# Performance work log

Hardware: AMD Instinct MI355X
Metric: run time of the kernel (lower is better)

The kernel has to match this reference:

```python
import jax, jax.numpy as jnp
import numpy as np

B, S, D = 32, 2048, 1024   # batch, seq, attention_in_dim
A = 1024                   # attention_dim
CTX = 1024                 # attention_context_dim
ADD = 256                  # additional decoder input dim
H = 1024                   # hidden_dim
OUT = 1024                 # output_dim
DEC_IN = 2 * D + ADD


def setup_inputs() -> dict:
    key = jax.random.key(0)
    ks = jax.random.split(key, 24)
    sc = 0.03
    inp = {
        "encoded_seq_ours": jax.random.normal(ks[0], (B, S, D), jnp.float32),
        "encoded_seq_ours_len": jax.random.randint(ks[1], (B,), 1, S + 1),
        "encoded_seq_theirs": jax.random.normal(ks[2], (B, S, D), jnp.float32),
        "encoded_seq_theirs_len": jax.random.randint(ks[3], (B,), 1, S + 1),
        "attention_context": jax.random.normal(ks[4], (B, CTX), jnp.float32),
        "additional_decoder_input": jax.random.normal(ks[5], (B, ADD), jnp.float32),
        "h0": jax.random.normal(ks[6], (B, H), jnp.float32),
        "c0": jax.random.normal(ks[7], (B, H), jnp.float32),
        "h1": jax.random.normal(ks[8], (B, H), jnp.float32),
        "c1": jax.random.normal(ks[9], (B, H), jnp.float32),
        "hidden_idx": jnp.arange(B, dtype=jnp.int32),
        # attention_theirs params (the module uses attention_theirs for BOTH calls)
        "att_Wh": jax.random.normal(ks[10], (A, D), jnp.float32) * sc,
        "att_Wc": jax.random.normal(ks[11], (A, CTX), jnp.float32) * sc,
        "att_v": jax.random.normal(ks[12], (1, A), jnp.float32) * sc,
        # LSTMCell layer 0
        "Wih0": jax.random.normal(ks[13], (4 * H, DEC_IN), jnp.float32) * sc,
        "Whh0": jax.random.normal(ks[14], (4 * H, H), jnp.float32) * sc,
        "bih0": jnp.zeros((4 * H,), jnp.float32),
        "bhh0": jnp.zeros((4 * H,), jnp.float32),
        # LSTMCell layer 1
        "Wih1": jax.random.normal(ks[15], (4 * H, H), jnp.float32) * sc,
        "Whh1": jax.random.normal(ks[16], (4 * H, H), jnp.float32) * sc,
        "bih1": jnp.zeros((4 * H,), jnp.float32),
        "bhh1": jnp.zeros((4 * H,), jnp.float32),
        # output linear (+ tanh activation)
        "Wout": jax.random.normal(ks[17], (OUT, H), jnp.float32) * sc,
        "bout": jnp.zeros((OUT,), jnp.float32),
    }
    return inp


def _attention(history, context, lengths, Wh, Wc, v):
    # history: [B,S,D], context: [B,CTX], lengths: [B]
    seq = history.shape[1]
    ha = jnp.einsum('bsd,ad->bsa', history, Wh)          # [B,S,A]
    ca = (context @ Wc.T)[:, None, :]                    # [B,1,A]
    score = jnp.einsum('bsa,oa->bso', jnp.tanh(ha + ca), v)  # [B,S,1]
    mask = (jnp.arange(seq) >= lengths[:, None])[:, :, None]  # [B,S,1] True = pad
    score = jnp.where(mask, -jnp.inf, score)
    score = jax.nn.softmax(score, axis=1)
    score = jnp.where(mask, 0.0, score)
    att = jnp.einsum('bs,bsd->bd', score[..., 0], history)    # [B,D]
    return att, score


def _lstm_cell(x, h, c, Wih, Whh, bih, bhh):
    gates = x @ Wih.T + h @ Whh.T + bih + bhh   # [B,4H]
    i, f, g, o = jnp.split(gates, 4, axis=-1)    # torch gate order: i,f,g,o
    i, f, o = jax.nn.sigmoid(i), jax.nn.sigmoid(f), jax.nn.sigmoid(o)
    g = jnp.tanh(g)
    c_new = f * c + i * g
    h_new = o * jnp.tanh(c_new)
    return h_new, c_new


def reference(encoded_seq_ours, encoded_seq_ours_len, encoded_seq_theirs,
              encoded_seq_theirs_len, attention_context, additional_decoder_input,
              h0, c0, h1, c1, hidden_idx,
              att_Wh, att_Wc, att_v,
              Wih0, Whh0, bih0, bhh0, Wih1, Whh1, bih1, bhh1, Wout, bout):
    # NOTE: original module uses attention_theirs for BOTH attention calls
    # (attention_ours is constructed but never used) -- reproduced faithfully.
    encoded_att_ours, scores_ours = _attention(
        encoded_seq_theirs, attention_context, encoded_seq_theirs_len,
        att_Wh, att_Wc, att_v)
    encoded_att_theirs, scores_theirs = _attention(
        encoded_seq_ours, attention_context, encoded_seq_ours_len,
        att_Wh, att_Wc, att_v)
    x = jnp.concatenate([encoded_att_ours, encoded_att_theirs,
                         additional_decoder_input], axis=-1)

    # layer 0 (dropout is eval-mode identity)
    h0_sel, c0_sel = h0[hidden_idx], c0[hidden_idx]
    h0_out, c0_out = _lstm_cell(x, h0_sel, c0_sel, Wih0, Whh0, bih0, bhh0)
    h0_new = h0.at[hidden_idx].set(h0_out)
    c0_new = c0.at[hidden_idx].set(c0_out)

    # layer 1
    h1_sel, c1_sel = h1[hidden_idx], c1[hidden_idx]
    h1_out, c1_out = _lstm_cell(h0_out, h1_sel, c1_sel, Wih1, Whh1, bih1, bhh1)
    h1_new = h1.at[hidden_idx].set(h1_out)
    c1_new = c1.at[hidden_idx].set(c1_out)

    out = jnp.tanh(h1_out @ Wout.T + bout)  # activation='tanh'
    return (out, h0_new, c0_new, h1_new, c1_new, scores_ours, scores_theirs)
```

## Files before the change

### kernel.cpp

```cpp
#include <hip/hip_runtime.h>
#include <hip/hip_bf16.h>

typedef __bf16 bf16x8 __attribute__((ext_vector_type(8)));
typedef float  f32x16 __attribute__((ext_vector_type(16)));
typedef unsigned short ushort_t;

#define B_   32
#define S_   2048
#define D_   1024
#define A_   1024
#define ADD_ 256
#define H_   1024

__device__ __forceinline__ float fast_rcp(float x){ return __builtin_amdgcn_rcpf(x); }
__device__ __forceinline__ float fast_sig(float x){ return fast_rcp(1.f + __expf(-x)); }
__device__ __forceinline__ float fast_tanh(float x){
  float ax = fabsf(x);
  float e  = __expf(-2.f * ax);
  float t  = (1.f - e) * fast_rcp(1.f + e);
  return copysignf(t, x);
}
__device__ __forceinline__ unsigned bfbits(float x){
  return (unsigned)__builtin_bit_cast(ushort_t, (__bf16)x);
}

__device__ __forceinline__ void stage16(const void* g, uint4* lds_base, int lane){
#if __has_builtin(__builtin_amdgcn_global_load_lds)
  __builtin_amdgcn_global_load_lds((const __attribute__((address_space(1))) void*)g,
                                   (__attribute__((address_space(3))) void*)lds_base,
                                   16, 0, 0);
#else
  lds_base[lane] = *reinterpret_cast<const uint4*>(g);
#endif
}

__global__ __launch_bounds__(256) void cvt8_k(const float* __restrict__ src,
                                              ushort_t* __restrict__ dst, int n8){
  int i = blockIdx.x * 256 + threadIdx.x;
  if (i >= n8) return;
  float4 a = reinterpret_cast<const float4*>(src)[i * 2];
  float4 b = reinterpret_cast<const float4*>(src)[i * 2 + 1];
  uint4 o;
  o.x = bfbits(a.x) | (bfbits(a.y) << 16);
  o.y = bfbits(a.z) | (bfbits(a.w) << 16);
  o.z = bfbits(b.x) | (bfbits(b.y) << 16);
  o.w = bfbits(b.z) | (bfbits(b.w) << 16);
  reinterpret_cast<uint4*>(dst)[i] = o;
}

template<bool PRECVT>
__global__ __launch_bounds__(256) void score_gemm(
    const float* __restrict__ hist_theirs, const float* __restrict__ hist_ours,
    const ushort_t* __restrict__ bfA, const ushort_t* __restrict__ whbf,
    const float* __restrict__ ca, const float* __restrict__ vvec,
    float* __restrict__ sraw){
  __shared__ uint4 As4[1024];
  __shared__ uint4 Bs4[1024];

  const int t  = threadIdx.x;
  const int bx = blockIdx.x;
  const int by = blockIdx.y;
  const int g  = by >> 4;
  const int b  = g & 31;
  const int srow0 = (by & 15) * 128;

  const int w = t >> 6, lane = t & 63;
  const int wr = w >> 1, wc = w & 1;
  const int l31 = lane & 31, lhi = lane >> 5;

  int Lrow[4], Ls[4];
  #pragma unroll
  for (int it = 0; it < 4; it++){
    int L = it * 256 + t;
    Lrow[it] = L >> 3;
    Ls[it]   = (L & 7) ^ ((L >> 3) & 7);
  }
  const ushort_t* bsrc[4];
  #pragma unroll
  for (int it = 0; it < 4; it++)
    bsrc[it] = whbf + (size_t)(bx * 128 + Lrow[it]) * D_ + Ls[it] * 8;

  const ushort_t* asrcb[4];
  const float* asrcf = nullptr; int sr = 0, sh = 0;
  if (PRECVT){
    #pragma unroll
    for (int it = 0; it < 4; it++)
      asrcb[it] = bfA + ((size_t)g * S_ + srow0 + Lrow[it]) * D_ + Ls[it] * 8;
  } else {
    sr = t >> 1; sh = t & 1;
    asrcf = ((g < 32) ? hist_theirs : hist_ours)
            + (size_t)b * S_ * D_ + (size_t)(srow0 + sr) * D_ + sh * 32;
  }

  f32x16 acc[2][2];
  #pragma unroll
  for (int m = 0; m < 2; m++)
    #pragma unroll
    for (int n = 0; n < 2; n++)
      #pragma unroll
      for (int i = 0; i < 16; i++) acc[m][n][i] = 0.f;

  for (int kc = 0; kc < D_; kc += 64) {
    if (PRECVT){
      #pragma unroll
      for (int it = 0; it < 4; it++)
        stage16(asrcb[it] + kc, &As4[it * 256 + w * 64], lane);
    } else {
      const float* p = asrcf + kc;
      float4 f[8];
      #pragma unroll
      for (int i = 0; i < 8; i++) f[i] = *reinterpret_cast<const float4*>(p + i * 4);
      #pragma unroll
      for (int j = 0; j < 4; j++) {
        bf16x8 o;
        float4 u = f[2 * j], v2 = f[2 * j + 1];
        o[0] = (__bf16)u.x;  o[1] = (__bf16)u.y;  o[2] = (__bf16)u.z;  o[3] = (__bf16)u.w;
        o[4] = (__bf16)v2.x; o[5] = (__bf16)v2.y; o[6] = (__bf16)v2.z; o[7] = (__bf16)v2.w;
        *reinterpret_cast<bf16x8*>(&As4[sr * 8 + ((sh * 4 + j) ^ (sr & 7))]) = o;
      }
    }
    #pragma unroll
    for (int it = 0; it < 4; it++)
      stage16(bsrc[it] + kc, &Bs4[it * 256 + w * 64], lane);
    __syncthreads();

    #pragma unroll
    for (int ks = 0; ks < 4; ks++) {
      bf16x8 af[2], bfr[2];
      #pragma unroll
      for (int m = 0; m < 2; m++) {
        int ar = wr * 64 + m * 32 + l31;
        af[m] = *reinterpret_cast<const bf16x8*>(&As4[ar * 8 + ((ks * 2 + lhi) ^ (ar & 7))]);
      }
      #pragma unroll
      for (int n = 0; n < 2; n++) {
        int br = wc * 64 + n * 32 + l31;
        bfr[n] = *reinterpret_cast<const bf16x8*>(&Bs4[br * 8 + ((ks * 2 + lhi) ^ (br & 7))]);
      }
      #pragma unroll
      for (int m = 0; m < 2; m++)
        #pragma unroll
        for (int n = 0; n < 2; n++)
          acc[m][n] = __builtin_amdgcn_mfma_f32_32x32x16_bf16(af[m], bfr[n], acc[m][n], 0, 0, 0);
    }
    __syncthreads();
  }

  float cav[2], vv[2];
  #pragma unroll
  for (int n = 0; n < 2; n++) {
    int col = bx * 128 + wc * 64 + n * 32 + l31;
    cav[n] = ca[b * A_ + col];
    vv[n]  = vvec[col];
  }
  #pragma unroll
  for (int m = 0; m < 2; m++) {
    float ts[16];
    #pragma unroll
    for (int r = 0; r < 16; r++) ts[r] = 0.f;
    #pragma unroll
    for (int n = 0; n < 2; n++)
      #pragma unroll
      for (int r = 0; r < 16; r++)
        ts[r] += fast_tanh(acc[m][n][r] + cav[n]) * vv[n];
    #pragma unroll
    for (int off = 1; off < 32; off <<= 1)
      #pragma unroll
      for (int r = 0; r < 16; r++)
        ts[r] += __shfl_xor(ts[r], off, 64);
    if (l31 == 0) {
      int rb = srow0 + wr * 64 + m * 32 + lhi * 4;
      #pragma unroll
      for (int r = 0; r < 16; r++) {
        int row = rb + (r & 3) + 8 * (r >> 2);
        atomicAdd(&sraw[(size_t)g * S_ + row], ts[r]);
      }
    }
  }
}

__global__ __launch_bounds__(256) void softmax_k(
    const float* __restrict__ sraw, const int* __restrict__ len_theirs,
    const int* __restrict__ len_ours, float* __restrict__ p, float* __restrict__ dout){
  const int g = blockIdx.x, t = threadIdx.x;
  const int len = (g < 32) ? len_theirs[g] : len_ours[g - 32];
  const float* row = sraw + (size_t)g * S_;
  float vals[8];
  #pragma unroll
  for (int i = 0; i < 8; i++) vals[i] = row[t * 8 + i];
  float mx = -1e30f;
  #pragma unroll
  for (int i = 0; i < 8; i++) if (t * 8 + i < len) mx = fmaxf(mx, vals[i]);
  #pragma unroll
  for (int off = 1; off < 64; off <<= 1) mx = fmaxf(mx, __shfl_xor(mx, off, 64));
  __shared__ float redm[4], reds[4];
  if ((t & 63) == 0) redm[t >> 6] = mx;
  __syncthreads();
  mx = fmaxf(fmaxf(redm[0], redm[1]), fmaxf(redm[2], redm[3]));
  float e[8]; float sum = 0.f;
  #pragma unroll
  for (int i = 0; i < 8; i++) {
    int s = t * 8 + i;
    e[i] = (s < len) ? __expf(vals[i] - mx) : 0.f;
    sum += e[i];
  }
  #pragma unroll
  for (int off = 1; off < 64; off <<= 1) sum += __shfl_xor(sum, off, 64);
  if ((t & 63) == 0) reds[t >> 6] = sum;
  __syncthreads();
  sum = reds[0] + reds[1] + reds[2] + reds[3];
  float rs = fast_rcp(sum);
  float* pd = p + (size_t)g * S_;
  float* od = (g < 32) ? (dout + 163840 + (size_t)g * S_)
                       : (dout + 229376 + (size_t)(g - 32) * S_);
  #pragma unroll
  for (int i = 0; i < 8; i++) {
    float pv = e[i] * rs;
    pd[t * 8 + i] = pv;
    od[t * 8 + i] = pv;
  }
}

__global__ __launch_bounds__(256) void att_k(
    const float* __restrict__ hist_theirs, const float* __restrict__ hist_ours,
    const float* __restrict__ p, float* __restrict__ att){
  const int g = blockIdx.x, ch = blockIdx.y, t = threadIdx.x;
  const float* hist = (g < 32 ? hist_theirs : hist_ours) + (size_t)(g & 31) * S_ * D_;
  const int s0 = ch * 128;
  __shared__ float ps[128];
  if (t < 128) ps[t] = p[(size_t)g * S_ + s0 + t];
  __syncthreads();
  float ax = 0.f, ay = 0.f, az = 0.f, aw = 0.f;
  const float* hp = hist + (size_t)s0 * D_ + t * 4;
  #pragma unroll 8
  for (int i = 0; i < 128; i++) {
    float4 hv = *reinterpret_cast<const float4*>(hp + (size_t)i * D_);
    float wgt = ps[i];
    ax += wgt * hv.x; ay += wgt * hv.y; az += wgt * hv.z; aw += wgt * hv.w;
  }
  float* ad = att + (size_t)g * D_ + t * 4;
  atomicAdd(ad + 0, ax); atomicAdd(ad + 1, ay);
  atomicAdd(ad + 2, az); atomicAdd(ad + 3, aw);
}

__global__ __launch_bounds__(256) void gemm_small(
    const float* __restrict__ X1, int ldx1, const float* __restrict__ W1, int K1,
    const float* __restrict__ X2, int ldx2, const float* __restrict__ W2, int K2,
    const float* __restrict__ b1, const float* __restrict__ b2,
    float* __restrict__ out, int ldo, int N, int act){
  const int lane = threadIdx.x & 63;
  const int wv   = blockIdx.x * 4 + (threadIdx.x >> 6);
  const int j0   = wv * 2;
  if (j0 >= N) return;
  float acc0[32], acc1[32];
  #pragma unroll
  for (int i = 0; i < 32; i++) { acc0[i] = 0.f; acc1[i] = 0.f; }
  {
    const float* w0p = W1 + (size_t)j0 * K1;
    const float* w1p = W1 + (size_t)(j0 + 1) * K1;
    for (int kc = lane * 4; kc < K1; kc += 256) {
      float4 w0 = *reinterpret_cast<const float4*>(w0p + kc);
      float4 w1 = *reinterpret_cast<const float4*>(w1p + kc);
      #pragma unroll
      for (int bb = 0; bb < 32; bb++) {
        float4 xv = *reinterpret_cast<const float4*>(X1 + (size_t)bb * ldx1 + kc);
        acc0[bb] += w0.x * xv.x + w0.y * xv.y + w0.z * xv.z + w0.w * xv.w;
        acc1[bb] += w1.x * xv.x + w1.y * xv.y + w1.z * xv.z + w1.w * xv.w;
      }
    }
  }
  if (W2) {
    const float* w0p = W2 + (size_t)j0 * K2;
    const float* w1p = W2 + (size_t)(j0 + 1) * K2;
    for (int kc = lane * 4; kc < K2; kc += 256) {
      float4 w0 = *reinterpret_cast<const float4*>(w0p + kc);
      float4 w1 = *reinterpret_cast<const float4*>(w1p + kc);
      #pragma unroll
      for (int bb = 0; bb < 32; bb++) {
        float4 xv = *reinterpret_cast<const float4*>(X2 + (size_t)bb * ldx2 + kc);
        acc0[bb] += w0.x * xv.x + w0.y * xv.y + w0.z * xv.z + w0.w * xv.w;
        acc1[bb] += w1.x * xv.x + w1.y * xv.y + w1.z * xv.z + w1.w * xv.w;
      }
    }
  }
  #pragma unroll
  for (int off = 1; off < 64; off <<= 1)
    #pragma unroll
    for (int bb = 0; bb < 32; bb++) {
      acc0[bb] += __shfl_xor(acc0[bb], off, 64);
      acc1[bb] += __shfl_xor(acc1[bb], off, 64);
    }
  float r0 = 0.f, r1 = 0.f;
  #pragma unroll
  for (int bb = 0; bb < 32; bb++) {
    if ((lane & 31) == bb) { r0 = acc0[bb]; r1 = acc1[bb]; }
  }
  if (lane < 32) {
    float bias0 = (b1 ? b1[j0] : 0.f) + (b2 ? b2[j0] : 0.f);
    float bias1 = (b1 ? b1[j0 + 1] : 0.f) + (b2 ? b2[j0 + 1] : 0.f);
    float v0 = r0 + bias0, v1 = r1 + bias1;
    if (act == 1) { v0 = fast_tanh(v0); v1 = fast_tanh(v1); }
    out[(size_t)lane * ldo + j0]     = v0;
    out[(size_t)lane * ldo + j0 + 1] = v1;
  }
}

__global__ __launch_bounds__(256) void buildx_k(
    const float* __restrict__ att, const float* __restrict__ addl,
    const float* __restrict__ h0, const int* __restrict__ idx, float* __restrict__ xc){
  const int b = blockIdx.y;
  const int k = blockIdx.x * 256 + threadIdx.x;
  if (k >= 3328) return;
  float v;
  if (k < 1024)      v = att[(size_t)b * D_ + k];
  else if (k < 2048) v = att[(size_t)(32 + b) * D_ + (k - 1024)];
  else if (k < 2304) v = addl[b * ADD_ + (k - 2048)];
  else               v = h0[(size_t)idx[b] * H_ + (k - 2304)];
  xc[(size_t)b * 3328 + k] = v;
}

__global__ __launch_bounds__(256) void lstm_pw(
    const float* __restrict__ gates, const float* __restrict__ c_prev,
    const int* __restrict__ idx, float* __restrict__ h_out, float* __restrict__ c_out,
    float* __restrict__ xc_next, int xld, const float* __restrict__ gather_src){
  const int b = blockIdx.y;
  const int h = blockIdx.x * 256 + threadIdx.x;
  const int ib = idx[b];
  const float gi = gates[(size_t)b * 4096 + h];
  const float gf = gates[(size_t)b * 4096 + 1024 + h];
  const float gg = gates[(size_t)b * 4096 + 2048 + h];
  const float go = gates[(size_t)b * 4096 + 3072 + h];
  const float cp = c_prev[(size_t)ib * H_ + h];
  const float i = fast_sig(gi), f = fast_sig(gf), o = fast_sig(go);
  const float gt = fast_tanh(gg);
  const float cn = f * cp + i * gt;
  const float hn = o * fast_tanh(cn);
  h_out[(size_t)ib * H_ + h] = hn;
  c_out[(size_t)ib * H_ + h] = cn;
  xc_next[(size_t)b * xld + h] = hn;
  if (gather_src) xc_next[(size_t)b * xld + H_ + h] = gather_src[(size_t)ib * H_ + h];
}

extern "C" void kernel_launch(void* const* d_in, const int* in_sizes, int n_in,
                              void* d_out, int out_size, void* d_ws, size_t ws_size,
                              hipStream_t stream){
  const float* seq_ours   = (const float*)d_in[0];
  const int*   len_ours   = (const int*)d_in[1];
  const float* seq_theirs = (const float*)d_in[2];
  const int*   len_theirs = (const int*)d_in[3];
  const float* ctx        = (const float*)d_in[4];
  const float* addl       = (const float*)d_in[5];
  const float* h0 = (const float*)d_in[6];
  const float* c0 = (const float*)d_in[7];
  const float* h1 = (const float*)d_in[8];
  const float* c1 = (const float*)d_in[9];
  const int*   idx = (const int*)d_in[10];
  const float* Wh  = (const float*)d_in[11];
  const float* Wc  = (const float*)d_in[12];
  const float* v   = (const float*)d_in[13];
  const float* Wih0 = (const float*)d_in[14];
  const float* Whh0 = (const float*)d_in[15];
  const float* bih0 = (const float*)d_in[16];
  const float* bhh0 = (const float*)d_in[17];
  const float* Wih1 = (const float*)d_in[18];
  const float* Whh1 = (const float*)d_in[19];
  const float* bih1 = (const float*)d_in[20];
  const float* bhh1 = (const float*)d_in[21];
  const float* Wout = (const float*)d_in[22];
  const float* bout = (const float*)d_in[23];

  float* out = (float*)d_out;
  char* ws = (char*)d_ws;
  float*    ca     = (float*)(ws + 0);
  float*    sraw   = (float*)(ws + 131072);
  float*    p      = (float*)(ws + 655360);
  float*    att    = (float*)(ws + 1179648);
  float*    xc     = (float*)(ws + 1441792);
  float*    gates0 = (float*)(ws + 1867776);
  float*    xc1    = (float*)(ws + 2392064);
  float*    gates1 = (float*)(ws + 2654208);
  float*    xc2    = (float*)(ws + 3178496);
  ushort_t* whbf   = (ushort_t*)(ws + 3309568);
  ushort_t* bfA    = (ushort_t*)(ws + 5406720);

  const size_t NEED = 5406720ull + 268435456ull;
  const bool precvt = ws_size >= NEED;

  hipMemsetAsync(sraw, 0, 64 * 2048 * 4, stream);
  hipMemsetAsync(att, 0, 64 * 1024 * 4, stream);
  cvt8_k<<<512, 256, 0, stream>>>(Wh, whbf, 131072);
  if (precvt){
    cvt8_k<<<32768, 256, 0, stream>>>(seq_theirs, bfA,            8388608);
    cvt8_k<<<32768, 256, 0, stream>>>(seq_ours,   bfA + 67108864, 8388608);
  }
  gemm_small<<<128, 256, 0, stream>>>(ctx, 1024, Wc, 1024, nullptr, 0, nullptr, 0,
                                      nullptr, nullptr, ca, 1024, 1024, 0);
  if (precvt)
    score_gemm<true><<<dim3(8, 1024), 256, 0, stream>>>(
        seq_theirs, seq_ours, bfA, whbf, ca, v, sraw);
  else
    score_gemm<false><<<dim3(8, 1024), 256, 0, stream>>>(
        seq_theirs, seq_ours, bfA, whbf, ca, v, sraw);
  softmax_k<<<64, 256, 0, stream>>>(sraw, len_theirs, len_ours, p, out);
  att_k<<<dim3(64, 16), 256, 0, stream>>>(seq_theirs, seq_ours, p, att);
  buildx_k<<<dim3(13, 32), 256, 0, stream>>>(att, addl, h0, idx, xc);
  gemm_small<<<512, 256, 0, stream>>>(xc, 3328, Wih0, 2304, xc + 2304, 3328, Whh0, 1024,
                                      bih0, bhh0, gates0, 4096, 4096, 0);
  lstm_pw<<<dim3(4, 32), 256, 0, stream>>>(gates0, c0, idx, out + 32768, out + 65536,
                                           xc1, 2048, h1);
  gemm_small<<<512, 256, 0, stream>>>(xc1, 2048, Wih1, 1024, xc1 + 1024, 2048, Whh1, 1024,
                                      bih1, bhh1, gates1, 4096, 4096, 0);
  lstm_pw<<<dim3(4, 32), 256, 0, stream>>>(gates1, c1, idx, out + 98304, out + 131072,
                                           xc2, 1024, nullptr);
  gemm_small<<<128, 256, 0, stream>>>(xc2, 1024, Wout, 1024, nullptr, 0, nullptr, 0,
                                      bout, nullptr, out, 1024, 1024, 1);
}
```

Baseline: 1.221 ms.

## Read bf16 history in attention-weighted sum, drop atomics, swizzle score GEMM blocks

The attention-weighted sum now reads the pre-converted bf16 copy of the encoder sequences instead of the fp32 originals, halving the bytes streamed. Results go to per-chunk partial buffers that buildx sums, replacing atomics and the memset. Separately, the score GEMM grid is flattened and remapped so neighbouring blocks share row tiles for better L2 reuse, and the convert kernel handles 16 elements per thread. The attention context now carries bf16 rounding error, and att_part reuses the whbf workspace region after the score GEMM has consumed it.

After: 1.126 ms. 1.08x faster.

```diff
diff --git a/kernel.cpp b/kernel.cpp
--- a/kernel.cpp
+++ b/kernel.cpp
@@ -23,6 +23,8 @@
 __device__ __forceinline__ unsigned bfbits(float x){
   return (unsigned)__builtin_bit_cast(ushort_t, (__bf16)x);
 }
+__device__ __forceinline__ float bf_lo(unsigned u){ return __builtin_bit_cast(float, u << 16); }
+__device__ __forceinline__ float bf_hi(unsigned u){ return __builtin_bit_cast(float, u & 0xffff0000u); }
 
 __device__ __forceinline__ void stage16(const void* g, uint4* lds_base, int lane){
 #if __has_builtin(__builtin_amdgcn_global_load_lds)
@@ -34,18 +36,23 @@
 #endif
 }
 
-__global__ __launch_bounds__(256) void cvt8_k(const float* __restrict__ src,
-                                              ushort_t* __restrict__ dst, int n8){
+__global__ __launch_bounds__(256) void cvt16_k(const float* __restrict__ src,
+                                               ushort_t* __restrict__ dst, int n16){
   int i = blockIdx.x * 256 + threadIdx.x;
-  if (i >= n8) return;
-  float4 a = reinterpret_cast<const float4*>(src)[i * 2];
-  float4 b = reinterpret_cast<const float4*>(src)[i * 2 + 1];
-  uint4 o;
-  o.x = bfbits(a.x) | (bfbits(a.y) << 16);
-  o.y = bfbits(a.z) | (bfbits(a.w) << 16);
-  o.z = bfbits(b.x) | (bfbits(b.y) << 16);
-  o.w = bfbits(b.z) | (bfbits(b.w) << 16);
-  reinterpret_cast<uint4*>(dst)[i] = o;
+  if (i >= n16) return;
+  const float4* s4 = reinterpret_cast<const float4*>(src) + (size_t)i * 4;
+  float4 a = s4[0], b = s4[1], c = s4[2], d = s4[3];
+  uint4 o0, o1;
+  o0.x = bfbits(a.x) | (bfbits(a.y) << 16);
+  o0.y = bfbits(a.z) | (bfbits(a.w) << 16);
+  o0.z = bfbits(b.x) | (bfbits(b.y) << 16);
+  o0.w = bfbits(b.z) | (bfbits(b.w) << 16);
+  o1.x = bfbits(c.x) | (bfbits(c.y) << 16);
+  o1.y = bfbits(c.z) | (bfbits(c.w) << 16);
+  o1.z = bfbits(d.x) | (bfbits(d.y) << 16);
+  o1.w = bfbits(d.z) | (bfbits(d.w) << 16);
+  uint4* dp = reinterpret_cast<uint4*>(dst) + (size_t)i * 2;
+  dp[0] = o0; dp[1] = o1;
 }
 
 template<bool PRECVT>
@@ -57,9 +64,10 @@
   __shared__ uint4 As4[1024];
   __shared__ uint4 Bs4[1024];
 
-  const int t  = threadIdx.x;
-  const int bx = blockIdx.x;
-  const int by = blockIdx.y;
+  const int t   = threadIdx.x;
+  const int bid = blockIdx.x;
+  const int bx  = (bid >> 3) & 7;
+  const int by  = ((bid >> 6) << 3) | (bid & 7);
   const int g  = by >> 4;
   const int b  = g & 31;
   const int srow0 = (by & 15) * 128;
@@ -221,26 +229,56 @@
   }
 }
 
+template<bool PRECVT>
 __global__ __launch_bounds__(256) void att_k(
     const float* __restrict__ hist_theirs, const float* __restrict__ hist_ours,
-    const float* __restrict__ p, float* __restrict__ att){
+    const ushort_t* __restrict__ bfA, const float* __restrict__ p,
+    float* __restrict__ att_part){
   const int g = blockIdx.x, ch = blockIdx.y, t = threadIdx.x;
-  const float* hist = (g < 32 ? hist_theirs : hist_ours) + (size_t)(g & 31) * S_ * D_;
-  const int s0 = ch * 128;
-  __shared__ float ps[128];
-  if (t < 128) ps[t] = p[(size_t)g * S_ + s0 + t];
+  const int s0 = ch * 256;
+  __shared__ float ps[256];
+  ps[t] = p[(size_t)g * S_ + s0 + t];
   __syncthreads();
-  float ax = 0.f, ay = 0.f, az = 0.f, aw = 0.f;
-  const float* hp = hist + (size_t)s0 * D_ + t * 4;
-  #pragma unroll 8
-  for (int i = 0; i < 128; i++) {
-    float4 hv = *reinterpret_cast<const float4*>(hp + (size_t)i * D_);
-    float wgt = ps[i];
-    ax += wgt * hv.x; ay += wgt * hv.y; az += wgt * hv.z; aw += wgt * hv.w;
-  }
-  float* ad = att + (size_t)g * D_ + t * 4;
-  atomicAdd(ad + 0, ax); atomicAdd(ad + 1, ay);
-  atomicAdd(ad + 2, az); atomicAdd(ad + 3, aw);
+  float* op = att_part + ((size_t)ch * 64 + g) * D_;
+  if (PRECVT){
+    __shared__ float red[128 * 8];
+    const int d0 = (t & 127) * 8;
+    const int sh = t >> 7;
+    const ushort_t* hp = bfA + ((size_t)g * S_ + s0 + sh * 128) * D_ + d0;
+    float acc[8];
+    #pragma unroll
+    for (int j = 0; j < 8; j++) acc[j] = 0.f;
+    #pragma unroll 4
+    for (int i = 0; i < 128; i++){
+      uint4 u = *reinterpret_cast<const uint4*>(hp + (size_t)i * D_);
+      float wgt = ps[sh * 128 + i];
+      acc[0] += wgt * bf_lo(u.x); acc[1] += wgt * bf_hi(u.x);
+      acc[2] += wgt * bf_lo(u.y); acc[3] += wgt * bf_hi(u.y);
+      acc[4] += wgt * bf_lo(u.z); acc[5] += wgt * bf_hi(u.z);
+      acc[6] += wgt * bf_lo(u.w); acc[7] += wgt * bf_hi(u.w);
+    }
+    if (sh == 1){
+      #pragma unroll
+      for (int j = 0; j < 8; j++) red[(t - 128) * 8 + j] = acc[j];
+    }
+    __syncthreads();
+    if (sh == 0){
+      #pragma unroll
+      for (int j = 0; j < 8; j++) op[d0 + j] = acc[j] + red[t * 8 + j];
+    }
+  } else {
+    const int d0 = t * 4;
+    const float* hist = (g < 32 ? hist_theirs : hist_ours) + (size_t)(g & 31) * S_ * D_;
+    const float* hp = hist + (size_t)s0 * D_ + d0;
+    float ax = 0.f, ay = 0.f, az = 0.f, aw = 0.f;
+    #pragma unroll 4
+    for (int i = 0; i < 256; i++){
+      float4 hv = *reinterpret_cast<const float4*>(hp + (size_t)i * D_);
+      float wgt = ps[i];
+      ax += wgt * hv.x; ay += wgt * hv.y; az += wgt * hv.z; aw += wgt * hv.w;
+    }
+    op[d0] = ax; op[d0 + 1] = ay; op[d0 + 2] = az; op[d0 + 3] = aw;
+  }
 }
 
 __global__ __launch_bounds__(256) void gemm_small(
@@ -306,14 +344,20 @@
 }
 
 __global__ __launch_bounds__(256) void buildx_k(
-    const float* __restrict__ att, const float* __restrict__ addl,
+    const float* __restrict__ att_part, const float* __restrict__ addl,
     const float* __restrict__ h0, const int* __restrict__ idx, float* __restrict__ xc){
   const int b = blockIdx.y;
   const int k = blockIdx.x * 256 + threadIdx.x;
   if (k >= 3328) return;
   float v;
-  if (k < 1024)      v = att[(size_t)b * D_ + k];
-  else if (k < 2048) v = att[(size_t)(32 + b) * D_ + (k - 1024)];
+  if (k < 2048) {
+    int g = (k < 1024) ? b : (32 + b);
+    int d = k & 1023;
+    v = 0.f;
+    #pragma unroll
+    for (int c = 0; c < 8; c++)
+      v += att_part[((size_t)c * 64 + g) * D_ + d];
+  }
   else if (k < 2304) v = addl[b * ADD_ + (k - 2048)];
   else               v = h0[(size_t)idx[b] * H_ + (k - 2304)];
   xc[(size_t)b * 3328 + k] = v;
@@ -374,36 +418,38 @@
   float*    ca     = (float*)(ws + 0);
   float*    sraw   = (float*)(ws + 131072);
   float*    p      = (float*)(ws + 655360);
-  float*    att    = (float*)(ws + 1179648);
   float*    xc     = (float*)(ws + 1441792);
   float*    gates0 = (float*)(ws + 1867776);
   float*    xc1    = (float*)(ws + 2392064);
   float*    gates1 = (float*)(ws + 2654208);
   float*    xc2    = (float*)(ws + 3178496);
   ushort_t* whbf   = (ushort_t*)(ws + 3309568);
+  float*    att_part = (float*)(ws + 3309568);
   ushort_t* bfA    = (ushort_t*)(ws + 5406720);
 
   const size_t NEED = 5406720ull + 268435456ull;
   const bool precvt = ws_size >= NEED;
 
   hipMemsetAsync(sraw, 0, 64 * 2048 * 4, stream);
-  hipMemsetAsync(att, 0, 64 * 1024 * 4, stream);
-  cvt8_k<<<512, 256, 0, stream>>>(Wh, whbf, 131072);
+  cvt16_k<<<256, 256, 0, stream>>>(Wh, whbf, 65536);
   if (precvt){
-    cvt8_k<<<32768, 256, 0, stream>>>(seq_theirs, bfA,            8388608);
-    cvt8_k<<<32768, 256, 0, stream>>>(seq_ours,   bfA + 67108864, 8388608);
+    cvt16_k<<<16384, 256, 0, stream>>>(seq_theirs, bfA,            4194304);
+    cvt16_k<<<16384, 256, 0, stream>>>(seq_ours,   bfA + 67108864, 4194304);
   }
   gemm_small<<<128, 256, 0, stream>>>(ctx, 1024, Wc, 1024, nullptr, 0, nullptr, 0,
                                       nullptr, nullptr, ca, 1024, 1024, 0);
   if (precvt)
-    score_gemm<true><<<dim3(8, 1024), 256, 0, stream>>>(
+    score_gemm<true><<<8192, 256, 0, stream>>>(
         seq_theirs, seq_ours, bfA, whbf, ca, v, sraw);
   else
-    score_gemm<false><<<dim3(8, 1024), 256, 0, stream>>>(
+    score_gemm<false><<<8192, 256, 0, stream>>>(
         seq_theirs, seq_ours, bfA, whbf, ca, v, sraw);
   softmax_k<<<64, 256, 0, stream>>>(sraw, len_theirs, len_ours, p, out);
-  att_k<<<dim3(64, 16), 256, 0, stream>>>(seq_theirs, seq_ours, p, att);
-  buildx_k<<<dim3(13, 32), 256, 0, stream>>>(att, addl, h0, idx, xc);
+  if (precvt)
+    att_k<true><<<dim3(64, 8), 256, 0, stream>>>(seq_theirs, seq_ours, bfA, p, att_part);
+  else
+    att_k<false><<<dim3(64, 8), 256, 0, stream>>>(seq_theirs, seq_ours, bfA, p, att_part);
+  buildx_k<<<dim3(13, 32), 256, 0, stream>>>(att_part, addl, h0, idx, xc);
   gemm_small<<<512, 256, 0, stream>>>(xc, 3328, Wih0, 2304, xc + 2304, 3328, Whh0, 1024,
                                       bih0, bhh0, gates0, 4096, 4096, 0);
   lstm_pw<<<dim3(4, 32), 256, 0, stream>>>(gates0, c0, idx, out + 32768, out + 65536,
```
